# Performance work log

Hardware: AMD Instinct MI355X
Metric: run time of the kernel (lower is better)

Reference implementation:

```python
import jax, jax.numpy as jnp
import numpy as np

# Hyperparams matching init_kwargs
KH = KW = KL = 3
SH = SW = SL = 1
PH = PW = PL = 1
DH = DW = DL = 1
DG = 1  # deformable_groups


def _out_dim(s, pad, dil, k, stride):
    return (s + 2 * pad - (dil * (k - 1) + 1)) // stride + 1


def _deform_conv3d(x, offset, mask, weight):
    # x: [N, C, H, W, L]; weight: [Cout, C//groups, KH, KW, KL] (groups=1)
    N, C, H, W, L = x.shape
    Cout = weight.shape[0]
    kprod = KH * KW * KL
    Ho = _out_dim(H, PH, DH, KH, SH)
    Wo = _out_dim(W, PW, DW, KW, SW)
    Lo = _out_dim(L, PL, DL, KL, SL)

    # offset layout: [N, DG, kprod, 3(h,w,l), Ho, Wo, Lo]; mask: [N, DG, kprod, Ho, Wo, Lo]
    off = offset.reshape(N, DG, kprod, 3, Ho, Wo, Lo)
    m = mask.reshape(N, DG, kprod, Ho, Wo, Lo)

    # kernel tap positions (kidx = i*KW*KL + j*KL + k), scaled by dilation
    ki, kj, kk = jnp.meshgrid(jnp.arange(KH), jnp.arange(KW), jnp.arange(KL), indexing='ij')
    kh = (ki.reshape(-1) * DH).astype(jnp.float32)  # [kprod]
    kw = (kj.reshape(-1) * DW).astype(jnp.float32)
    kl = (kk.reshape(-1) * DL).astype(jnp.float32)

    hb = (jnp.arange(Ho) * SH - PH).astype(jnp.float32)
    wb = (jnp.arange(Wo) * SW - PW).astype(jnp.float32)
    lb = (jnp.arange(Lo) * SL - PL).astype(jnp.float32)

    # sampling coordinates: [N, DG, kprod, Ho, Wo, Lo]
    ch = off[:, :, :, 0] + hb[None, None, None, :, None, None] + kh[None, None, :, None, None, None]
    cw = off[:, :, :, 1] + wb[None, None, None, None, :, None] + kw[None, None, :, None, None, None]
    cl = off[:, :, :, 2] + lb[None, None, None, None, None, :] + kl[None, None, :, None, None, None]

    Cpg = C // DG
    xf = x.reshape(N, DG, Cpg, H * W * L)
    P = kprod * Ho * Wo * Lo

    h0 = jnp.floor(ch); w0 = jnp.floor(cw); l0 = jnp.floor(cl)
    fh = ch - h0; fw = cw - w0; fl = cl - l0
    h0i = h0.astype(jnp.int32); w0i = w0.astype(jnp.int32); l0i = l0.astype(jnp.int32)

    # trilinear interpolation: accumulate over 8 corners (zero outside volume)
    val = jnp.zeros((N, DG, Cpg, P), x.dtype)
    for dh in (0, 1):
        for dw in (0, 1):
            for dl in (0, 1):
                ih = h0i + dh; iw = w0i + dw; il = l0i + dl
                wgt = (fh if dh else 1.0 - fh) * (fw if dw else 1.0 - fw) * (fl if dl else 1.0 - fl)
                valid = (ih >= 0) & (ih < H) & (iw >= 0) & (iw < W) & (il >= 0) & (il < L)
                lin = ((jnp.clip(ih, 0, H - 1) * W + jnp.clip(iw, 0, W - 1)) * L
                       + jnp.clip(il, 0, L - 1)).reshape(N, DG, 1, P)
                g = jnp.take_along_axis(xf, jnp.broadcast_to(lin, (N, DG, Cpg, P)), axis=3)
                val = val + g * (wgt * valid).reshape(N, DG, 1, P)

    # modulate by mask, then contract columns with weight (groups=1)
    val = val.reshape(N, DG, Cpg, kprod, Ho, Wo, Lo) * m[:, :, None]
    cols = val.reshape(N, C, kprod, Ho * Wo * Lo)
    out = jnp.einsum('nckp,ock->nop', cols, weight.reshape(Cout, C, kprod))
    return out.reshape(N, Cout, Ho, Wo, Lo)


def setup_inputs() -> dict:
    key = jax.random.key(0)
    k1, k2, k3, k4 = jax.random.split(key, 4)
    N, C, H, W, L = 1, 64, 32, 32, 32
    Cout = 64
    kprod = KH * KW * KL
    Ho = _out_dim(H, PH, DH, KH, SH)
    Wo = _out_dim(W, PW, DW, KW, SW)
    Lo = _out_dim(L, PL, DL, KL, SL)
    x = jax.random.normal(k1, (N, C, H, W, L), jnp.float32)
    offset = jax.random.normal(k2, (N, DG * 3 * kprod, Ho, Wo, Lo), jnp.float32)
    mask = jax.random.uniform(k3, (N, DG * kprod, Ho, Wo, Lo), jnp.float32)
    stdv = 1.0 / np.sqrt(C * kprod)
    weight = jax.random.uniform(k4, (Cout, C, KH, KW, KL), jnp.float32, -stdv, stdv)
    return {"x": x, "offset": offset, "mask": mask, "weight": weight}


def reference(x, offset, mask, weight):
    return _deform_conv3d(x, offset, mask, weight)
```

## Files before the change

kernel.cpp:

```cpp
#include <hip/hip_runtime.h>
#include <hip/hip_bf16.h>

typedef short short8 __attribute__((ext_vector_type(8)));
typedef unsigned int u32x4 __attribute__((ext_vector_type(4)));
typedef float f32x4 __attribute__((ext_vector_type(4)));
typedef float f32x2 __attribute__((ext_vector_type(2)));

#define SPAT  32768
#define KPROD 27

static __device__ __forceinline__ short f2bf(float f) {
    return (short)__bfloat16_as_ushort(__float2bfloat16(f));
}

__global__ void transpose_x_bf16(const float* __restrict__ x, unsigned short* __restrict__ xt) {
    __shared__ float tile[64][65];
    const int t = threadIdx.x;
    const int s0 = blockIdx.x * 64;
    const int lane = t & 63, grp = t >> 6;
#pragma unroll
    for (int r = 0; r < 16; ++r) {
        int c = grp * 16 + r;
        tile[c][lane] = x[c * SPAT + s0 + lane];
    }
    __syncthreads();
#pragma unroll
    for (int r = 0; r < 16; ++r) {
        int srow = grp * 16 + r;
        xt[(s0 + srow) * 64 + lane] = __bfloat16_as_ushort(__float2bfloat16(tile[lane][srow]));
    }
}

__global__ void prep_w_frag(const float* __restrict__ w, unsigned short* __restrict__ wt) {
    int idx = blockIdx.x * 256 + threadIdx.x;
    if (idx >= KPROD * 4096) return;
    int k = idx >> 12;
    int fid = idx & 4095;
    int i = fid >> 9;
    int lane = (fid >> 3) & 63;
    int e = fid & 7;
    int ot = i >> 1, kb = i & 1;
    int o = ot * 16 + (lane & 15);
    int c = kb * 32 + (lane >> 4) * 8 + e;
    wt[idx] = __bfloat16_as_ushort(__float2bfloat16(w[(o * 64 + c) * KPROD + k]));
}

__global__ __launch_bounds__(128)
void dconv3d_quad(const unsigned short* __restrict__ xt, const unsigned short* __restrict__ wf,
                  const float* __restrict__ offset, const float* __restrict__ mask,
                  float* __restrict__ out) {
    __shared__ float meta_w[2][2][8][24];
    __shared__ int   meta_o[2][2][8][24];
    __shared__ float red[16][65];

    const int t    = threadIdx.x;
    const int wid  = t >> 6;
    const int l    = t & 63;
    const int pl   = l & 15;
    const int g    = l >> 4;
    const int gp   = l >> 2;
    const int gg   = l & 3;
    const int goff = wid * 64 + gg * 16;
    const int bpidx = (pl * 4 + g) * 4;

    const int nwg = (int)gridDim.x;
    const int cpx = nwg >> 3;
    const int bid = (int)blockIdx.x;
    const int bsw = (bid & 7) * cpx + (bid >> 3);

    const int p_base = bsw * 16;
    const int pos = p_base + pl;
    const int ho = pos >> 10, wo = (pos >> 5) & 31, lo = pos & 31;
    const char* xbase = (const char*)xt;

    f32x4 acc[4] = {};

    auto compute_meta = [&](int k, int buf) {
        float oh = offset[(3 * k + 0) * SPAT + pos];
        float ow = offset[(3 * k + 1) * SPAT + pos];
        float ol = offset[(3 * k + 2) * SPAT + pos];
        float mk = mask[k * SPAT + pos];
        int ki = k / 9, kj = (k / 3) % 3, kk2 = k % 3;
        float chh = oh + (float)(ho - 1 + ki);
        float cww = ow + (float)(wo - 1 + kj);
        float cll = ol + (float)(lo - 1 + kk2);
        float h0f = floorf(chh), w0f = floorf(cww), l0f = floorf(cll);
        float fh = chh - h0f, fw = cww - w0f, fl = cll - l0f;
        int h0 = (int)h0f, w0 = (int)w0f, l0i = (int)l0f;
#pragma unroll
        for (int jj = 0; jj < 2; ++jj) {
            int j = g * 2 + jj;
            int dh = j >> 2, dw = (j >> 1) & 1, dl = j & 1;
            int ih = h0 + dh, iw = w0 + dw, il = l0i + dl;
            float wh = dh ? fh : 1.f - fh;
            float ww = dw ? fw : 1.f - fw;
            float wl = dl ? fl : 1.f - fl;
            bool valid = (unsigned)ih < 32u && (unsigned)iw < 32u && (unsigned)il < 32u;
            float wvv = valid ? wh * ww * wl * mk : 0.f;
            int ihc = min(max(ih, 0), 31);
            int iwc = min(max(iw, 0), 31);
            int ilc = min(max(il, 0), 31);
            int lin = (ihc * 32 + iwc) * 32 + ilc;
            meta_w[wid][buf][j][pl] = wvv;
            meta_o[wid][buf][j][pl] = lin * 128;
        }
    };

    compute_meta(0, 0);
    u32x4 q[8];
#pragma unroll
    for (int j = 0; j < 8; ++j)
        q[j] = *(const u32x4*)(xbase + (meta_o[wid][0][j][gp] + goff));

#pragma unroll 1
    for (int k = 0; k < KPROD; ++k) {
        const int buf  = k & 1;
        const int bufn = buf ^ 1;

        if (k + 1 < KPROD) compute_meta(k + 1, bufn);

        short8 wfr[4];
#pragma unroll
        for (int ot = 0; ot < 4; ++ot)
            wfr[ot] = *(const short8*)&wf[((size_t)k * 8 + ot * 2 + wid) * 512 + l * 8];

        f32x2 v[4] = {};
#pragma unroll
        for (int j = 0; j < 8; ++j) {
            float w = meta_w[wid][buf][j][gp];
            f32x2 w2 = {w, w};
#pragma unroll
            for (int qd = 0; qd < 4; ++qd) {
                unsigned int a = q[j][qd];
                f32x2 xa = {__uint_as_float(a << 16), __uint_as_float(a & 0xffff0000u)};
                v[qd] = __builtin_elementwise_fma(w2, xa, v[qd]);
            }
        }

        union { short8 s; u32x4 u; } bg;
#pragma unroll
        for (int qd = 0; qd < 4; ++qd) {
            bg.s[2*qd]   = f2bf(v[qd].x);
            bg.s[2*qd+1] = f2bf(v[qd].y);
        }

        if (k + 1 < KPROD) {
#pragma unroll
            for (int j = 0; j < 8; ++j)
                q[j] = *(const u32x4*)(xbase + (meta_o[wid][bufn][j][gp] + goff));
        }

        union { u32x4 u; short8 s; } bm;
#pragma unroll
        for (int d = 0; d < 4; ++d)
            bm.u[d] = (unsigned)__builtin_amdgcn_ds_bpermute(bpidx, (int)bg.u[d]);

        __builtin_amdgcn_s_setprio(1);
#pragma unroll
        for (int ot = 0; ot < 4; ++ot)
            acc[ot] = __builtin_amdgcn_mfma_f32_16x16x32_bf16(wfr[ot], bm.s, acc[ot], 0, 0, 0);
        __builtin_amdgcn_s_setprio(0);
    }

    __syncthreads();
    if (wid == 0) {
#pragma unroll
        for (int ot = 0; ot < 4; ++ot)
#pragma unroll
            for (int r = 0; r < 4; ++r)
                red[pl][ot * 16 + g * 4 + r] = acc[ot][r];
    }
    __syncthreads();
    if (wid == 1) {
#pragma unroll
        for (int ot = 0; ot < 4; ++ot)
#pragma unroll
            for (int r = 0; r < 4; ++r)
                red[pl][ot * 16 + g * 4 + r] += acc[ot][r];
    }
    __syncthreads();

#pragma unroll
    for (int it = 0; it < 8; ++it) {
        int idx = it * 128 + t;
        int p = idx & 15, o = idx >> 4;
        out[(size_t)o * SPAT + p_base + p] = red[p][o];
    }
}

extern "C" void kernel_launch(void* const* d_in, const int* in_sizes, int n_in,
                              void* d_out, int out_size, void* d_ws, size_t ws_size,
                              hipStream_t stream) {
    const float* x      = (const float*)d_in[0];
    const float* offset = (const float*)d_in[1];
    const float* mask   = (const float*)d_in[2];
    const float* weight = (const float*)d_in[3];
    float* out = (float*)d_out;

    unsigned short* xt  = (unsigned short*)d_ws;
    unsigned short* wtb = (unsigned short*)((char*)d_ws + (size_t)SPAT * 64 * 2);

    hipLaunchKernelGGL(transpose_x_bf16, dim3(SPAT / 64), dim3(256), 0, stream, x, xt);
    hipLaunchKernelGGL(prep_w_frag, dim3((KPROD * 4096 + 255) / 256), dim3(256), 0, stream,
                       weight, wtb);
    hipLaunchKernelGGL(dconv3d_quad, dim3(SPAT / 16), dim3(128), 0, stream,
                       xt, wtb, offset, mask, out);
}
```

Measured before the change: 84.53 us.

## Prefetch offsets two taps ahead and pack per-corner sampling metadata

Offset and mask values are now loaded two kernel taps ahead into registers, so their global-load latency overlaps the current tap's gather and MFMA work. Sampling metadata (weight plus byte offset) is packed into one f32x2 LDS entry, and each 4-lane group computes the h/w corner pair and both l-neighbours together, sharing the common weight factors. Metadata for the next tap is read into registers once and reused for both the gather addresses and the interpolation weights. This costs extra registers for the prefetched values and may reduce occupancy.

```diff
diff --git a/kernel.cpp b/kernel.cpp
--- a/kernel.cpp
+++ b/kernel.cpp
@@ -46,11 +46,10 @@
 }
 
 __global__ __launch_bounds__(128)
-void dconv3d_quad(const unsigned short* __restrict__ xt, const unsigned short* __restrict__ wf,
+void dconv3d_pipe(const unsigned short* __restrict__ xt, const unsigned short* __restrict__ wf,
                   const float* __restrict__ offset, const float* __restrict__ mask,
                   float* __restrict__ out) {
-    __shared__ float meta_w[2][2][8][24];
-    __shared__ int   meta_o[2][2][8][24];
+    __shared__ f32x2 meta[2][2][8][17];
     __shared__ float red[16][65];
 
     const int t    = threadIdx.x;
@@ -58,6 +57,7 @@
     const int l    = t & 63;
     const int pl   = l & 15;
     const int g    = l >> 4;
+    const int dh   = g >> 1, dw = g & 1;
     const int gp   = l >> 2;
     const int gg   = l & 3;
     const int goff = wid * 64 + gg * 16;
@@ -71,53 +71,73 @@
     const int p_base = bsw * 16;
     const int pos = p_base + pl;
     const int ho = pos >> 10, wo = (pos >> 5) & 31, lo = pos & 31;
+    const float fho = (float)(ho - 1), fwo = (float)(wo - 1), flo = (float)(lo - 1);
     const char* xbase = (const char*)xt;
 
     f32x4 acc[4] = {};
 
-    auto compute_meta = [&](int k, int buf) {
-        float oh = offset[(3 * k + 0) * SPAT + pos];
-        float ow = offset[(3 * k + 1) * SPAT + pos];
-        float ol = offset[(3 * k + 2) * SPAT + pos];
-        float mk = mask[k * SPAT + pos];
+    auto load_off = [&](int k) -> f32x4 {
+        f32x4 r;
+        r.x = offset[(3 * k + 0) * SPAT + pos];
+        r.y = offset[(3 * k + 1) * SPAT + pos];
+        r.z = offset[(3 * k + 2) * SPAT + pos];
+        r.w = mask[k * SPAT + pos];
+        return r;
+    };
+
+    auto compute_meta = [&](int k, int buf, f32x4 om) {
         int ki = k / 9, kj = (k / 3) % 3, kk2 = k % 3;
-        float chh = oh + (float)(ho - 1 + ki);
-        float cww = ow + (float)(wo - 1 + kj);
-        float cll = ol + (float)(lo - 1 + kk2);
+        float chh = om.x + (fho + (float)ki);
+        float cww = om.y + (fwo + (float)kj);
+        float cll = om.z + (flo + (float)kk2);
         float h0f = floorf(chh), w0f = floorf(cww), l0f = floorf(cll);
         float fh = chh - h0f, fw = cww - w0f, fl = cll - l0f;
         int h0 = (int)h0f, w0 = (int)w0f, l0i = (int)l0f;
-#pragma unroll
-        for (int jj = 0; jj < 2; ++jj) {
-            int j = g * 2 + jj;
-            int dh = j >> 2, dw = (j >> 1) & 1, dl = j & 1;
-            int ih = h0 + dh, iw = w0 + dw, il = l0i + dl;
-            float wh = dh ? fh : 1.f - fh;
-            float ww = dw ? fw : 1.f - fw;
-            float wl = dl ? fl : 1.f - fl;
-            bool valid = (unsigned)ih < 32u && (unsigned)iw < 32u && (unsigned)il < 32u;
-            float wvv = valid ? wh * ww * wl * mk : 0.f;
-            int ihc = min(max(ih, 0), 31);
-            int iwc = min(max(iw, 0), 31);
-            int ilc = min(max(il, 0), 31);
-            int lin = (ihc * 32 + iwc) * 32 + ilc;
-            meta_w[wid][buf][j][pl] = wvv;
-            meta_o[wid][buf][j][pl] = lin * 128;
-        }
+        int ih = h0 + dh, iw = w0 + dw;
+        float wh = dh ? fh : 1.f - fh;
+        float ww = dw ? fw : 1.f - fw;
+        float whwm = wh * ww * om.w;
+        float w1v = whwm * fl;
+        float w0v = whwm - w1v;
+        bool vhw = ((unsigned)ih < 32u) && ((unsigned)iw < 32u);
+        bool v0 = vhw && ((unsigned)l0i < 32u);
+        bool v1 = vhw && ((unsigned)(l0i + 1) < 32u);
+        w0v = v0 ? w0v : 0.f;
+        w1v = v1 ? w1v : 0.f;
+        int ihc = min(max(ih, 0), 31), iwc = min(max(iw, 0), 31);
+        int l0c = min(max(l0i, 0), 31);
+        int l1c = min(max(l0i + 1, 0), 31);
+        int base2 = (ihc * 32 + iwc) * 32;
+        f32x2 m0, m1;
+        m0.x = w0v; m0.y = __int_as_float((base2 + l0c) << 7);
+        m1.x = w1v; m1.y = __int_as_float((base2 + l1c) << 7);
+        meta[wid][buf][2 * g][pl]     = m0;
+        meta[wid][buf][2 * g + 1][pl] = m1;
     };
 
-    compute_meta(0, 0);
+    f32x4 offA = load_off(0);
+    compute_meta(0, 0, offA);
+    offA = load_off(1);
+    float mw[8]; int mo[8];
+#pragma unroll
+    for (int j = 0; j < 8; ++j) {
+        f32x2 md = meta[wid][0][j][gp];
+        mw[j] = md.x; mo[j] = __float_as_int(md.y);
+    }
     u32x4 q[8];
 #pragma unroll
     for (int j = 0; j < 8; ++j)
-        q[j] = *(const u32x4*)(xbase + (meta_o[wid][0][j][gp] + goff));
+        q[j] = *(const u32x4*)(xbase + (mo[j] + goff));
 
 #pragma unroll 1
     for (int k = 0; k < KPROD; ++k) {
         const int buf  = k & 1;
         const int bufn = buf ^ 1;
 
-        if (k + 1 < KPROD) compute_meta(k + 1, bufn);
+        f32x4 offB;
+        if (k + 2 < KPROD) offB = load_off(k + 2);
+
+        if (k + 1 < KPROD) compute_meta(k + 1, bufn, offA);
 
         short8 wfr[4];
 #pragma unroll
@@ -127,8 +147,7 @@
         f32x2 v[4] = {};
 #pragma unroll
         for (int j = 0; j < 8; ++j) {
-            float w = meta_w[wid][buf][j][gp];
-            f32x2 w2 = {w, w};
+            f32x2 w2 = {mw[j], mw[j]};
 #pragma unroll
             for (int qd = 0; qd < 4; ++qd) {
                 unsigned int a = q[j][qd];
@@ -136,18 +155,22 @@
                 v[qd] = __builtin_elementwise_fma(w2, xa, v[qd]);
             }
         }
-
         union { short8 s; u32x4 u; } bg;
 #pragma unroll
         for (int qd = 0; qd < 4; ++qd) {
-            bg.s[2*qd]   = f2bf(v[qd].x);
-            bg.s[2*qd+1] = f2bf(v[qd].y);
+            bg.s[2 * qd]     = f2bf(v[qd].x);
+            bg.s[2 * qd + 1] = f2bf(v[qd].y);
         }
 
         if (k + 1 < KPROD) {
 #pragma unroll
+            for (int j = 0; j < 8; ++j) {
+                f32x2 md = meta[wid][bufn][j][gp];
+                mw[j] = md.x; mo[j] = __float_as_int(md.y);
+            }
+#pragma unroll
             for (int j = 0; j < 8; ++j)
-                q[j] = *(const u32x4*)(xbase + (meta_o[wid][bufn][j][gp] + goff));
+                q[j] = *(const u32x4*)(xbase + (mo[j] + goff));
         }
 
         union { u32x4 u; short8 s; } bm;
@@ -160,6 +183,8 @@
         for (int ot = 0; ot < 4; ++ot)
             acc[ot] = __builtin_amdgcn_mfma_f32_16x16x32_bf16(wfr[ot], bm.s, acc[ot], 0, 0, 0);
         __builtin_amdgcn_s_setprio(0);
+
+        offA = offB;
     }
 
     __syncthreads();
@@ -203,6 +228,6 @@
     hipLaunchKernelGGL(transpose_x_bf16, dim3(SPAT / 64), dim3(256), 0, stream, x, xt);
     hipLaunchKernelGGL(prep_w_frag, dim3((KPROD * 4096 + 255) / 256), dim3(256), 0, stream,
                        weight, wtb);
-    hipLaunchKernelGGL(dconv3d_quad, dim3(SPAT / 16), dim3(128), 0, stream,
+    hipLaunchKernelGGL(dconv3d_pipe, dim3(SPAT / 16), dim3(128), 0, stream,
                        xt, wtb, offset, mask, out);
 }
```

Result: no change. 83.91 us (-0.7%).
